# Kernel optimization log

Hardware: AMD Instinct MI355X
Metric: run time of the kernel (lower is better)

Reference implementation:

```python
import jax, jax.numpy as jnp
import numpy as np

D_MODEL = 1024
NUM_HEADS = 16
D_HEAD = D_MODEL // NUM_HEADS


def setup_inputs() -> dict:
    key = jax.random.key(0)
    kx, kq, kk, kv, ko = jax.random.split(key, 5)
    scale = 1.0 / np.sqrt(D_MODEL)
    X = jax.random.normal(kx, (4, 2048, D_MODEL), dtype=jnp.float32)
    # nn.Linear weights stored as [out, in]; we keep that convention.
    W_Q = jax.random.uniform(kq, (D_MODEL, D_MODEL), jnp.float32, -scale, scale)
    W_K = jax.random.uniform(kk, (D_MODEL, D_MODEL), jnp.float32, -scale, scale)
    W_V = jax.random.uniform(kv, (D_MODEL, D_MODEL), jnp.float32, -scale, scale)
    W_O = jax.random.uniform(ko, (D_MODEL, D_MODEL), jnp.float32, -scale, scale)
    return {"X": X, "W_Q": W_Q, "W_K": W_K, "W_V": W_V, "W_O": W_O}


def reference(X, W_Q, W_K, W_V, W_O):
    B, S, D = X.shape
    H, Dh = NUM_HEADS, D_HEAD
    # projections (Linear: x @ W.T)
    Q = (X @ W_Q.T).reshape(B, S, H, Dh).transpose(0, 2, 1, 3)  # [B,H,S,Dh]
    K = (X @ W_K.T).reshape(B, S, H, Dh).transpose(0, 2, 1, 3)
    V = (X @ W_V.T).reshape(B, S, H, Dh).transpose(0, 2, 1, 3)
    scores = jnp.einsum('bhqd,bhkd->bhqk', Q, K) / jnp.sqrt(jnp.float32(Dh))
    causal = jnp.tril(jnp.ones((S, S), dtype=bool))  # True = keep
    scores = jnp.where(causal, scores, -jnp.inf)
    attn = jax.nn.softmax(scores, axis=-1)
    out = jnp.einsum('bhqk,bhkd->bhqd', attn, V)  # [B,H,S,Dh]
    out = out.transpose(0, 2, 1, 3).reshape(B, S, D)
    return out @ W_O.T
```

## Files before the change

### kernel.cpp

```cpp
#include <hip/hip_runtime.h>

#define S_LEN 2048
#define NH 16
#define DH 64
#define DM 1024
#define M_TOK 8192
#define SZX ((size_t)M_TOK * DM)
#define SZW ((size_t)DM * DM)

typedef unsigned short u16;
typedef unsigned int u32;
typedef __attribute__((ext_vector_type(8))) short bf16x8;
typedef __attribute__((ext_vector_type(4))) float f32x4;

__device__ __forceinline__ u16 f2bf(float f) {
  union { float f; u32 u; } v; v.f = f;
  return (u16)((v.u + 0x8000u) >> 16);
}
__device__ __forceinline__ u32 pack_bf2(float x, float y) {
  union { float f; u32 u; } a, b; a.f = x; b.f = y;
  return __builtin_amdgcn_perm(b.u + 0x8000u, a.u + 0x8000u, 0x07060302u);
}
__device__ __forceinline__ float fast_exp2(float x) {
  float r; asm("v_exp_f32 %0, %1" : "=v"(r) : "v"(x)); return r;
}
__device__ __forceinline__ void gload16(const u16* g, u16* l) {
  __builtin_amdgcn_global_load_lds((const __attribute__((address_space(1))) void*)g,
                                   (__attribute__((address_space(3))) void*)l,
                                   16, 0, 0);
}

#define QSCALE 0.18033688f

__global__ __launch_bounds__(256) void cast_all(const float* __restrict__ X,
                                                const float* __restrict__ q,
                                                const float* __restrict__ k,
                                                const float* __restrict__ v,
                                                const float* __restrict__ o,
                                                u16* __restrict__ dst) {
  const int i = (blockIdx.x * 256 + threadIdx.x) * 8;
  const float* src;
  int local;
  if (i < (int)SZX) { src = X; local = i; }
  else {
    const int j = i - (int)SZX;
    const int region = j >> 20;
    src = (region == 0) ? q : (region == 1) ? k : (region == 2) ? v : o;
    local = j & ((1 << 20) - 1);
  }
  const float4 a = *(const float4*)(src + local);
  const float4 b = *(const float4*)(src + local + 4);
  uint4 r;
  r.x = pack_bf2(a.x, a.y); r.y = pack_bf2(a.z, a.w);
  r.z = pack_bf2(b.x, b.y); r.w = pack_bf2(b.z, b.w);
  *(uint4*)(dst + i) = r;
}

template<int MODE>
__global__ __launch_bounds__(256) void gemm128(const u16* __restrict__ A,
                                               const u16* __restrict__ Bw,
                                               void* __restrict__ Cv) {
  __shared__ __align__(16) u16 As[128 * 64];
  __shared__ __align__(16) u16 Bs[128 * 64];
  const int tid = threadIdx.x;
  const int lane = tid & 63;
  const int wave = tid >> 6;
  const int col = lane & 15, quad = lane >> 4;
  const int wm = (wave & 1) * 64, wn = (wave >> 1) * 64;
  const int m_blk = blockIdx.x * 128, n_blk = blockIdx.y * 128;

  const int srow = tid >> 3;
  const int skg = (tid & 7) ^ (srow & 7);
  const u16* Ag = A + (size_t)(m_blk + srow) * DM + skg * 8;
  const u16* Bg = Bw + (size_t)(n_blk + srow) * DM + skg * 8;

  f32x4 acc[4][4];
#pragma unroll
  for (int i = 0; i < 4; ++i)
#pragma unroll
    for (int j = 0; j < 4; ++j) acc[i][j] = (f32x4){0.f, 0.f, 0.f, 0.f};

  const int c0 = (quad ^ (col & 7)) * 8;
  const int c1 = c0 ^ 32;

  for (int k0 = 0; k0 < DM; k0 += 64) {
#pragma unroll
    for (int i = 0; i < 4; ++i) {
      gload16(Ag + (size_t)(32 * i) * DM + k0, &As[tid * 8 + i * 2048]);
      gload16(Bg + (size_t)(32 * i) * DM + k0, &Bs[tid * 8 + i * 2048]);
    }
    __syncthreads();
    bf16x8 af[4], bf[4];
#pragma unroll
    for (int i = 0; i < 4; ++i)
      af[i] = *(const bf16x8*)&As[(wm + i * 16 + col) * 64 + c0];
#pragma unroll
    for (int j = 0; j < 4; ++j)
      bf[j] = *(const bf16x8*)&Bs[(wn + j * 16 + col) * 64 + c0];
#pragma unroll
    for (int i = 0; i < 4; ++i)
#pragma unroll
      for (int j = 0; j < 4; ++j)
        acc[i][j] = __builtin_amdgcn_mfma_f32_16x16x32_bf16(af[i], bf[j], acc[i][j], 0, 0, 0);
#pragma unroll
    for (int i = 0; i < 4; ++i)
      af[i] = *(const bf16x8*)&As[(wm + i * 16 + col) * 64 + c1];
#pragma unroll
    for (int j = 0; j < 4; ++j)
      bf[j] = *(const bf16x8*)&Bs[(wn + j * 16 + col) * 64 + c1];
#pragma unroll
    for (int i = 0; i < 4; ++i)
#pragma unroll
      for (int j = 0; j < 4; ++j)
        acc[i][j] = __builtin_amdgcn_mfma_f32_16x16x32_bf16(af[i], bf[j], acc[i][j], 0, 0, 0);
    __syncthreads();
  }

#pragma unroll
  for (int i = 0; i < 4; ++i) {
#pragma unroll
    for (int j = 0; j < 4; ++j) {
      const int n = n_blk + wn + j * 16 + col;
      if (MODE == 0) {
        const int which = n >> 10;
        const int nn = n & 1023;
        const int h = nn >> 6, dh = nn & 63;
        u16* dst = (u16*)Cv + (size_t)which * SZX;
        const int m0 = m_blk + wm + i * 16 + quad * 4;
        const int b = m0 >> 11;
        if (which == 2) {
          uint2 pk;
          pk.x = pack_bf2(acc[i][j][0], acc[i][j][1]);
          pk.y = pack_bf2(acc[i][j][2], acc[i][j][3]);
          *(uint2*)&dst[((size_t)((b * NH + h) * DH + dh)) * S_LEN + (m0 & 2047)] = pk;
        } else {
          const float sc = (which == 0) ? QSCALE : 1.0f;
#pragma unroll
          for (int r = 0; r < 4; ++r) {
            const int m = m0 + r, s = m & 2047;
            dst[((size_t)(b * NH + h) * S_LEN + s) * DH + dh] = f2bf(acc[i][j][r] * sc);
          }
        }
      } else {
#pragma unroll
        for (int r = 0; r < 4; ++r) {
          const int m = m_blk + wm + i * 16 + quad * 4 + r;
          ((float*)Cv)[(size_t)m * DM + n] = acc[i][j][r];
        }
      }
    }
  }
}

template<bool DIAG_H, bool DIAG_L, bool WITH_L>
__device__ __forceinline__ void stepHL(const u16* __restrict__ Ksb,
                                       const u16* __restrict__ Vsb,
                                       u16* __restrict__ Pw,
                                       bf16x8 qH0, bf16x8 qH1,
                                       bf16x8 qL0, bf16x8 qL1,
                                       f32x4& lH, f32x4* oH,
                                       f32x4& lL, f32x4* oL,
                                       f32x4 zero4, bf16x8 ones,
                                       int c0, int c1, int col, int quad,
                                       int q_l) {
  const int colc = col & 7;
  f32x4 sH[4], sL[4];
#pragma unroll
  for (int t = 0; t < 4; ++t) {
    const int row = (t * 16 + col) * 64;
    const bf16x8 kf0 = *(const bf16x8*)&Ksb[row + c0];
    const bf16x8 kf1 = *(const bf16x8*)&Ksb[row + c1];
    f32x4 z = __builtin_amdgcn_mfma_f32_16x16x32_bf16(kf0, qH0, zero4, 0, 0, 0);
    sH[t] = __builtin_amdgcn_mfma_f32_16x16x32_bf16(kf1, qH1, z, 0, 0, 0);
    if (WITH_L) {
      f32x4 y = __builtin_amdgcn_mfma_f32_16x16x32_bf16(kf0, qL0, zero4, 0, 0, 0);
      sL[t] = __builtin_amdgcn_mfma_f32_16x16x32_bf16(kf1, qL1, y, 0, 0, 0);
    }
  }
#pragma unroll
  for (int t = 0; t < 4; ++t)
#pragma unroll
    for (int r = 0; r < 4; ++r) {
      if (DIAG_H && (t * 16 + quad * 4 + r) > q_l) sH[t][r] = -1e30f;
      sH[t][r] = fast_exp2(sH[t][r]);
      if (WITH_L) {
        if (DIAG_L && (t * 16 + quad * 4 + r) > q_l) sL[t][r] = -1e30f;
        sL[t][r] = fast_exp2(sL[t][r]);
      }
    }
#pragma unroll
  for (int t = 0; t < 4; ++t) {
    uint2 pk;
    pk.x = pack_bf2(sH[t][0], sH[t][1]);
    pk.y = pack_bf2(sH[t][2], sH[t][3]);
    const int pg = (((t * 2) + (quad >> 1)) ^ colc) * 8 + (quad & 1) * 4;
    *(uint2*)&Pw[col * 64 + pg] = pk;
  }
  {
    const bf16x8 pf0 = *(const bf16x8*)&Pw[col * 64 + ((quad ^ colc) * 8)];
    const bf16x8 pf1 = *(const bf16x8*)&Pw[col * 64 + (((4 + quad) ^ colc) * 8)];
    lH = __builtin_amdgcn_mfma_f32_16x16x32_bf16(ones, pf0, lH, 0, 0, 0);
    lH = __builtin_amdgcn_mfma_f32_16x16x32_bf16(ones, pf1, lH, 0, 0, 0);
#pragma unroll
    for (int t = 0; t < 4; ++t) {
      const int row = (t * 16 + col) * 64;
      const bf16x8 vf0 = *(const bf16x8*)&Vsb[row + c0];
      const bf16x8 vf1 = *(const bf16x8*)&Vsb[row + c1];
      oH[t] = __builtin_amdgcn_mfma_f32_16x16x32_bf16(vf0, pf0, oH[t], 0, 0, 0);
      oH[t] = __builtin_amdgcn_mfma_f32_16x16x32_bf16(vf1, pf1, oH[t], 0, 0, 0);
    }
  }
  if (WITH_L) {
#pragma unroll
    for (int t = 0; t < 4; ++t) {
      uint2 pk;
      pk.x = pack_bf2(sL[t][0], sL[t][1]);
      pk.y = pack_bf2(sL[t][2], sL[t][3]);
      const int pg = (((t * 2) + (quad >> 1)) ^ colc) * 8 + (quad & 1) * 4;
      *(uint2*)&Pw[col * 64 + pg] = pk;
    }
    const bf16x8 pf0 = *(const bf16x8*)&Pw[col * 64 + ((quad ^ colc) * 8)];
    const bf16x8 pf1 = *(const bf16x8*)&Pw[col * 64 + (((4 + quad) ^ colc) * 8)];
    lL = __builtin_amdgcn_mfma_f32_16x16x32_bf16(ones, pf0, lL, 0, 0, 0);
    lL = __builtin_amdgcn_mfma_f32_16x16x32_bf16(ones, pf1, lL, 0, 0, 0);
#pragma unroll
    for (int t = 0; t < 4; ++t) {
      const int row = (t * 16 + col) * 64;
      const bf16x8 vf0 = *(const bf16x8*)&Vsb[row + c0];
      const bf16x8 vf1 = *(const bf16x8*)&Vsb[row + c1];
      oL[t] = __builtin_amdgcn_mfma_f32_16x16x32_bf16(vf0, pf0, oL[t], 0, 0, 0);
      oL[t] = __builtin_amdgcn_mfma_f32_16x16x32_bf16(vf1, pf1, oL[t], 0, 0, 0);
    }
  }
}

__global__ __launch_bounds__(256) void attn_kernel(const u16* __restrict__ Qg,
                                                   const u16* __restrict__ Kg,
                                                   const u16* __restrict__ Vtg,
                                                   u16* __restrict__ AO) {
  __shared__ __align__(16) u16 Ks[2][64 * 64];
  __shared__ __align__(16) u16 Vs[2][64 * 64];
  __shared__ __align__(16) u16 Ps[4][16 * 64];

  const int id = blockIdx.x;
  const int k9 = id >> 3;
  const int qtH = 16 + (k9 & 15);
  const int qtL = 31 - qtH;
  const int bh = ((id & 7) << 3) | (k9 >> 4);
  const int tid = threadIdx.x, lane = tid & 63, wave = tid >> 6;
  const int col = lane & 15, quad = lane >> 4;

  const u16* Qb = Qg + (size_t)bh * S_LEN * DH;
  const u16* Kb = Kg + (size_t)bh * S_LEN * DH;
  const u16* Vb = Vtg + (size_t)bh * DH * S_LEN;

  const u16* qrowH = Qb + (size_t)(qtH * 64 + wave * 16 + col) * DH + quad * 8;
  const u16* qrowL = Qb + (size_t)(qtL * 64 + wave * 16 + col) * DH + quad * 8;
  const bf16x8 qH0 = *(const bf16x8*)(qrowH);
  const bf16x8 qH1 = *(const bf16x8*)(qrowH + 32);
  const bf16x8 qL0 = *(const bf16x8*)(qrowL);
  const bf16x8 qL1 = *(const bf16x8*)(qrowL + 32);

  const f32x4 zero4 = (f32x4){0.f, 0.f, 0.f, 0.f};
  const bf16x8 ones = (bf16x8){0x3F80, 0x3F80, 0x3F80, 0x3F80,
                               0x3F80, 0x3F80, 0x3F80, 0x3F80};

  f32x4 lH = zero4, lL = zero4;
  f32x4 oH[4], oL[4];
#pragma unroll
  for (int t = 0; t < 4; ++t) { oH[t] = zero4; oL[t] = zero4; }

  const int sr0 = tid >> 3;
  const int sk0 = (tid & 7) ^ (sr0 & 7);
  const u16* K0 = Kb + (size_t)sr0 * DH + sk0 * 8;
  const u16* K1 = Kb + (size_t)(sr0 + 32) * DH + sk0 * 8;
  const u16* V0 = Vb + (size_t)sr0 * S_LEN + sk0 * 8;
  const u16* V1 = Vb + (size_t)(sr0 + 32) * S_LEN + sk0 * 8;

  const int c0 = (quad ^ (col & 7)) * 8;
  const int c1 = c0 ^ 32;
  const int q_l = wave * 16 + col;
  u16* Pw = &Ps[wave][0];

  gload16(K0, &Ks[0][tid * 8]);
  gload16(K1, &Ks[0][2048 + tid * 8]);
  gload16(V0, &Vs[0][tid * 8]);
  gload16(V1, &Vs[0][2048 + tid * 8]);

#define PREFETCH(nk) do {                                   \
    const int nb_ = (nk) & 1;                               \
    gload16(K0 + (size_t)(nk) * 64 * DH, &Ks[nb_][tid * 8]);\
    gload16(K1 + (size_t)(nk) * 64 * DH, &Ks[nb_][2048 + tid * 8]); \
    gload16(V0 + (nk) * 64, &Vs[nb_][tid * 8]);             \
    gload16(V1 + (nk) * 64, &Vs[nb_][2048 + tid * 8]);      \
  } while (0)

  int kt = 0;
  for (; kt < qtL; ++kt) {
    __syncthreads();
    PREFETCH(kt + 1);
    stepHL<false, false, true>(&Ks[kt & 1][0], &Vs[kt & 1][0], Pw,
                               qH0, qH1, qL0, qL1, lH, oH, lL, oL,
                               zero4, ones, c0, c1, col, quad, q_l);
  }
  {
    __syncthreads();
    PREFETCH(kt + 1);
    stepHL<false, true, true>(&Ks[kt & 1][0], &Vs[kt & 1][0], Pw,
                              qH0, qH1, qL0, qL1, lH, oH, lL, oL,
                              zero4, ones, c0, c1, col, quad, q_l);
    ++kt;
  }
  for (; kt < qtH; ++kt) {
    __syncthreads();
    PREFETCH(kt + 1);
    stepHL<false, false, false>(&Ks[kt & 1][0], &Vs[kt & 1][0], Pw,
                                qH0, qH1, qL0, qL1, lH, oH, lL, oL,
                                zero4, ones, c0, c1, col, quad, q_l);
  }
  {
    __syncthreads();
    stepHL<true, false, false>(&Ks[kt & 1][0], &Vs[kt & 1][0], Pw,
                               qH0, qH1, qL0, qL1, lH, oH, lL, oL,
                               zero4, ones, c0, c1, col, quad, q_l);
  }
#undef PREFETCH

  const int b = bh >> 4, h = bh & 15;
  {
    const float inv = __builtin_amdgcn_rcpf(lH[0]);
    const size_t base = (size_t)(b * S_LEN + qtH * 64 + q_l) * DM + h * DH;
#pragma unroll
    for (int t = 0; t < 4; ++t) {
      uint2 pk;
      pk.x = pack_bf2(oH[t][0] * inv, oH[t][1] * inv);
      pk.y = pack_bf2(oH[t][2] * inv, oH[t][3] * inv);
      *(uint2*)&AO[base + t * 16 + quad * 4] = pk;
    }
  }
  {
    const float inv = __builtin_amdgcn_rcpf(lL[0]);
    const size_t base = (size_t)(b * S_LEN + qtL * 64 + q_l) * DM + h * DH;
#pragma unroll
    for (int t = 0; t < 4; ++t) {
      uint2 pk;
      pk.x = pack_bf2(oL[t][0] * inv, oL[t][1] * inv);
      pk.y = pack_bf2(oL[t][2] * inv, oL[t][3] * inv);
      *(uint2*)&AO[base + t * 16 + quad * 4] = pk;
    }
  }
}

extern "C" void kernel_launch(void* const* d_in, const int* in_sizes, int n_in,
                              void* d_out, int out_size, void* d_ws, size_t ws_size,
                              hipStream_t stream) {
  const float* X  = (const float*)d_in[0];
  const float* Wq = (const float*)d_in[1];
  const float* Wk = (const float*)d_in[2];
  const float* Wv = (const float*)d_in[3];
  const float* Wo = (const float*)d_in[4];

  u16* Xb   = (u16*)d_ws;
  u16* Wqkv = Xb + SZX;
  u16* Wob  = Wqkv + 3 * SZW;
  u16* Qb   = Wob + SZW;
  u16* Kb   = Qb + SZX;
  u16* VT   = Kb + SZX;
  u16* AO   = Xb;

  cast_all<<<(int)((SZX + 4 * SZW) / 8 / 256), 256, 0, stream>>>(X, Wq, Wk, Wv, Wo, Xb);

  gemm128<0><<<dim3(M_TOK / 128, 3 * DM / 128), 256, 0, stream>>>(Xb, Wqkv, Qb);

  attn_kernel<<<dim3(1024), 256, 0, stream>>>(Qb, Kb, VT, AO);

  gemm128<1><<<dim3(M_TOK / 128, DM / 128), 256, 0, stream>>>(AO, Wob, d_out);
}
```

Measured before the change: 245.5 us.

## Add 256x256 double-buffered 8-wave GEMM for fused QKV projection

Replaces the 128x128 tile QKV projection GEMM with a new 256x256 tile kernel using 512 threads. It double-buffers LDS and interleaves global-to-LDS staging with four MFMA sub-phases under s_setprio. The larger tile raises arithmetic intensity and cuts global traffic, and the software pipeline is meant to hide load latency. In exchange it uses 128KB of LDS per block and heavy register pressure, and it launches only 384 blocks, which may hurt occupancy and load balance.

```diff
diff --git a/kernel.cpp b/kernel.cpp
--- a/kernel.cpp
+++ b/kernel.cpp
@@ -7,6 +7,7 @@
 #define M_TOK 8192
 #define SZX ((size_t)M_TOK * DM)
 #define SZW ((size_t)DM * DM)
+#define NT 16
 
 typedef unsigned short u16;
 typedef unsigned int u32;
@@ -54,6 +55,154 @@
   r.x = pack_bf2(a.x, a.y); r.y = pack_bf2(a.z, a.w);
   r.z = pack_bf2(b.x, b.y); r.w = pack_bf2(b.z, b.w);
   *(uint4*)(dst + i) = r;
+}
+
+template<int QM, int QN>
+__device__ __forceinline__ void mm_phase(f32x4 (&acc)[8][4],
+                                         const bf16x8 (&A)[4][2],
+                                         const bf16x8 (&B)[2][2]) {
+  __builtin_amdgcn_s_setprio(1);
+#pragma unroll
+  for (int i = 0; i < 4; ++i)
+#pragma unroll
+    for (int j = 0; j < 2; ++j) {
+      f32x4& d = acc[QM * 4 + i][QN * 2 + j];
+      d = __builtin_amdgcn_mfma_f32_16x16x32_bf16(A[i][0], B[j][0], d, 0, 0, 0);
+      d = __builtin_amdgcn_mfma_f32_16x16x32_bf16(A[i][1], B[j][1], d, 0, 0, 0);
+    }
+  __builtin_amdgcn_s_setprio(0);
+}
+
+__global__ __launch_bounds__(512, 2) void gemm256_qkv(const u16* __restrict__ A,
+                                                      const u16* __restrict__ Bw,
+                                                      u16* __restrict__ Cv) {
+  __shared__ __align__(16) u16 As[2][256 * 64];
+  __shared__ __align__(16) u16 Bs[2][256 * 64];
+  const int tid = threadIdx.x;
+  const int lane = tid & 63;
+  const int wave = tid >> 6;
+  const int col = lane & 15, quad = lane >> 4;
+  const int wr = wave >> 2;
+  const int wc = wave & 3;
+  const int m_blk = blockIdx.x * 256, n_blk = blockIdx.y * 256;
+
+  const int srow = tid >> 3;
+  const int skg = (tid & 7) ^ (srow & 7);
+  const int lofs = tid * 8;
+  const u16* Ag = A + (size_t)(m_blk + srow) * DM + skg * 8;
+  const u16* Bg = Bw + (size_t)(n_blk + srow) * DM + skg * 8;
+
+  f32x4 acc[8][4];
+#pragma unroll
+  for (int i = 0; i < 8; ++i)
+#pragma unroll
+    for (int j = 0; j < 4; ++j) acc[i][j] = (f32x4){0.f, 0.f, 0.f, 0.f};
+
+  const int c0 = (quad ^ (col & 7)) * 8;
+  const int c1 = c0 ^ 32;
+
+#define STG_A(hm, tt) do {                                                   \
+    gload16(Ag + (size_t)((hm) * 128) * DM + (tt) * 64,                      \
+            &As[(tt) & 1][(hm) * 8192 + lofs]);                              \
+    gload16(Ag + (size_t)((hm) * 128 + 64) * DM + (tt) * 64,                 \
+            &As[(tt) & 1][(hm) * 8192 + 4096 + lofs]);                       \
+  } while (0)
+#define STG_B(hn, tt) do {                                                   \
+    gload16(Bg + (size_t)((hn) * 128) * DM + (tt) * 64,                      \
+            &Bs[(tt) & 1][(hn) * 8192 + lofs]);                              \
+    gload16(Bg + (size_t)((hn) * 128 + 64) * DM + (tt) * 64,                 \
+            &Bs[(tt) & 1][(hn) * 8192 + 4096 + lofs]);                       \
+  } while (0)
+
+  STG_A(0, 0); STG_B(0, 0); STG_A(1, 0); STG_B(1, 0);
+  STG_A(0, 1); STG_B(0, 1);
+  asm volatile("s_waitcnt vmcnt(4)" ::: "memory");
+  __builtin_amdgcn_s_barrier();
+
+  bf16x8 af[4][2], bq0[2][2], bq1[2][2];
+
+  for (int t = 0; t < NT; ++t) {
+    const u16* Ab = As[t & 1];
+    const u16* Bb = Bs[t & 1];
+
+#pragma unroll
+    for (int i = 0; i < 4; ++i) {
+      const int ro = (wr * 64 + i * 16 + col) * 64;
+      af[i][0] = *(const bf16x8*)&Ab[ro + c0];
+      af[i][1] = *(const bf16x8*)&Ab[ro + c1];
+    }
+#pragma unroll
+    for (int j = 0; j < 2; ++j) {
+      const int ro = (wc * 32 + j * 16 + col) * 64;
+      bq0[j][0] = *(const bf16x8*)&Bb[ro + c0];
+      bq0[j][1] = *(const bf16x8*)&Bb[ro + c1];
+    }
+    if (t + 1 < NT) STG_A(1, t + 1);
+    __builtin_amdgcn_s_barrier();
+    asm volatile("s_waitcnt lgkmcnt(0)" ::: "memory");
+    mm_phase<0, 0>(acc, af, bq0);
+    __builtin_amdgcn_s_barrier();
+
+#pragma unroll
+    for (int j = 0; j < 2; ++j) {
+      const int ro = (128 + wc * 32 + j * 16 + col) * 64;
+      bq1[j][0] = *(const bf16x8*)&Bb[ro + c0];
+      bq1[j][1] = *(const bf16x8*)&Bb[ro + c1];
+    }
+    if (t + 1 < NT) STG_B(1, t + 1);
+    __builtin_amdgcn_s_barrier();
+    asm volatile("s_waitcnt lgkmcnt(0)" ::: "memory");
+    mm_phase<0, 1>(acc, af, bq1);
+    __builtin_amdgcn_s_barrier();
+
+#pragma unroll
+    for (int i = 0; i < 4; ++i) {
+      const int ro = (128 + wr * 64 + i * 16 + col) * 64;
+      af[i][0] = *(const bf16x8*)&Ab[ro + c0];
+      af[i][1] = *(const bf16x8*)&Ab[ro + c1];
+    }
+    if (t + 2 < NT) STG_A(0, t + 2);
+    __builtin_amdgcn_s_barrier();
+    asm volatile("s_waitcnt lgkmcnt(0)" ::: "memory");
+    mm_phase<1, 0>(acc, af, bq0);
+    __builtin_amdgcn_s_barrier();
+
+    if (t + 2 < NT) STG_B(0, t + 2);
+    __builtin_amdgcn_s_barrier();
+    mm_phase<1, 1>(acc, af, bq1);
+    if (t < NT - 2) { asm volatile("s_waitcnt vmcnt(4)" ::: "memory"); }
+    else            { asm volatile("s_waitcnt vmcnt(0)" ::: "memory"); }
+    __builtin_amdgcn_s_barrier();
+  }
+#undef STG_A
+#undef STG_B
+
+  const int which = n_blk >> 10;
+#pragma unroll
+  for (int mi = 0; mi < 8; ++mi) {
+#pragma unroll
+    for (int nj = 0; nj < 4; ++nj) {
+      const int n = n_blk + (nj >> 1) * 128 + wc * 32 + (nj & 1) * 16 + col;
+      const int nn = n & 1023;
+      const int h = nn >> 6, dh = nn & 63;
+      u16* dst = Cv + (size_t)which * SZX;
+      const int m0 = m_blk + (mi >> 2) * 128 + wr * 64 + (mi & 3) * 16 + quad * 4;
+      const int b = m0 >> 11;
+      if (which == 2) {
+        uint2 pk;
+        pk.x = pack_bf2(acc[mi][nj][0], acc[mi][nj][1]);
+        pk.y = pack_bf2(acc[mi][nj][2], acc[mi][nj][3]);
+        *(uint2*)&dst[((size_t)((b * NH + h) * DH + dh)) * S_LEN + (m0 & 2047)] = pk;
+      } else {
+        const float sc = (which == 0) ? QSCALE : 1.0f;
+#pragma unroll
+        for (int r = 0; r < 4; ++r) {
+          const int m = m0 + r, s = m & 2047;
+          dst[((size_t)(b * NH + h) * S_LEN + s) * DH + dh] = f2bf(acc[mi][nj][r] * sc);
+        }
+      }
+    }
+  }
 }
 
 template<int MODE>
@@ -370,7 +519,7 @@
 
   cast_all<<<(int)((SZX + 4 * SZW) / 8 / 256), 256, 0, stream>>>(X, Wq, Wk, Wv, Wo, Xb);
 
-  gemm128<0><<<dim3(M_TOK / 128, 3 * DM / 128), 256, 0, stream>>>(Xb, Wqkv, Qb);
+  gemm256_qkv<<<dim3(M_TOK / 256, 3 * DM / 256), 512, 0, stream>>>(Xb, Wqkv, Qb);
 
   attn_kernel<<<dim3(1024), 256, 0, stream>>>(Qb, Kb, VT, AO);
 
```

After: 255.0 us. 3.8% more time.

## Pair adjacent query tiles per K/V stream, two pairs per block

Applied to the files above, without the earlier changes.

Each attention block now processes two pairs of adjacent query tiles (2p, 2p+1), taken from mirrored positions so the causal work is balanced. The two tiles in a pair share nearly the whole K/V stream, so each loaded K/V tile feeds both query tiles, and the lower tile is fully masked only on the final step. The grid is halved to 512 blocks. The old H/L pairing (qtH, 31-qtH) also shared K/V across the lower tile's prefix. The new layout aims for better MFMA interleaving (H and L PV MFMAs are now issued together), at the cost of fewer blocks and a serialized second pass per block.

```diff
diff --git a/kernel.cpp b/kernel.cpp
--- a/kernel.cpp
+++ b/kernel.cpp
@@ -152,17 +152,17 @@
   }
 }
 
-template<bool DIAG_H, bool DIAG_L, bool WITH_L>
-__device__ __forceinline__ void stepHL(const u16* __restrict__ Ksb,
-                                       const u16* __restrict__ Vsb,
-                                       u16* __restrict__ Pw,
-                                       bf16x8 qH0, bf16x8 qH1,
-                                       bf16x8 qL0, bf16x8 qL1,
-                                       f32x4& lH, f32x4* oH,
-                                       f32x4& lL, f32x4* oL,
-                                       f32x4 zero4, bf16x8 ones,
-                                       int c0, int c1, int col, int quad,
-                                       int q_l) {
+template<bool DIAG_L>
+__device__ __forceinline__ void stepM(const u16* __restrict__ Ksb,
+                                      const u16* __restrict__ Vsb,
+                                      u16* __restrict__ Pw,
+                                      bf16x8 qH0, bf16x8 qH1,
+                                      bf16x8 qL0, bf16x8 qL1,
+                                      f32x4& lH, f32x4* oH,
+                                      f32x4& lL, f32x4* oL,
+                                      f32x4 zero4, bf16x8 ones,
+                                      int c0, int c1, int col, int quad,
+                                      int q_l) {
   const int colc = col & 7;
   f32x4 sH[4], sL[4];
 #pragma unroll
@@ -172,21 +172,16 @@
     const bf16x8 kf1 = *(const bf16x8*)&Ksb[row + c1];
     f32x4 z = __builtin_amdgcn_mfma_f32_16x16x32_bf16(kf0, qH0, zero4, 0, 0, 0);
     sH[t] = __builtin_amdgcn_mfma_f32_16x16x32_bf16(kf1, qH1, z, 0, 0, 0);
-    if (WITH_L) {
-      f32x4 y = __builtin_amdgcn_mfma_f32_16x16x32_bf16(kf0, qL0, zero4, 0, 0, 0);
-      sL[t] = __builtin_amdgcn_mfma_f32_16x16x32_bf16(kf1, qL1, y, 0, 0, 0);
-    }
+    f32x4 y = __builtin_amdgcn_mfma_f32_16x16x32_bf16(kf0, qL0, zero4, 0, 0, 0);
+    sL[t] = __builtin_amdgcn_mfma_f32_16x16x32_bf16(kf1, qL1, y, 0, 0, 0);
   }
 #pragma unroll
   for (int t = 0; t < 4; ++t)
 #pragma unroll
     for (int r = 0; r < 4; ++r) {
-      if (DIAG_H && (t * 16 + quad * 4 + r) > q_l) sH[t][r] = -1e30f;
       sH[t][r] = fast_exp2(sH[t][r]);
-      if (WITH_L) {
-        if (DIAG_L && (t * 16 + quad * 4 + r) > q_l) sL[t][r] = -1e30f;
-        sL[t][r] = fast_exp2(sL[t][r]);
-      }
+      if (DIAG_L && (t * 16 + quad * 4 + r) > q_l) sL[t][r] = -1e30f;
+      sL[t][r] = fast_exp2(sL[t][r]);
     }
 #pragma unroll
   for (int t = 0; t < 4; ++t) {
@@ -196,41 +191,79 @@
     const int pg = (((t * 2) + (quad >> 1)) ^ colc) * 8 + (quad & 1) * 4;
     *(uint2*)&Pw[col * 64 + pg] = pk;
   }
-  {
-    const bf16x8 pf0 = *(const bf16x8*)&Pw[col * 64 + ((quad ^ colc) * 8)];
-    const bf16x8 pf1 = *(const bf16x8*)&Pw[col * 64 + (((4 + quad) ^ colc) * 8)];
-    lH = __builtin_amdgcn_mfma_f32_16x16x32_bf16(ones, pf0, lH, 0, 0, 0);
-    lH = __builtin_amdgcn_mfma_f32_16x16x32_bf16(ones, pf1, lH, 0, 0, 0);
-#pragma unroll
-    for (int t = 0; t < 4; ++t) {
-      const int row = (t * 16 + col) * 64;
-      const bf16x8 vf0 = *(const bf16x8*)&Vsb[row + c0];
-      const bf16x8 vf1 = *(const bf16x8*)&Vsb[row + c1];
-      oH[t] = __builtin_amdgcn_mfma_f32_16x16x32_bf16(vf0, pf0, oH[t], 0, 0, 0);
-      oH[t] = __builtin_amdgcn_mfma_f32_16x16x32_bf16(vf1, pf1, oH[t], 0, 0, 0);
-    }
-  }
-  if (WITH_L) {
-#pragma unroll
-    for (int t = 0; t < 4; ++t) {
-      uint2 pk;
-      pk.x = pack_bf2(sL[t][0], sL[t][1]);
-      pk.y = pack_bf2(sL[t][2], sL[t][3]);
-      const int pg = (((t * 2) + (quad >> 1)) ^ colc) * 8 + (quad & 1) * 4;
-      *(uint2*)&Pw[col * 64 + pg] = pk;
-    }
-    const bf16x8 pf0 = *(const bf16x8*)&Pw[col * 64 + ((quad ^ colc) * 8)];
-    const bf16x8 pf1 = *(const bf16x8*)&Pw[col * 64 + (((4 + quad) ^ colc) * 8)];
-    lL = __builtin_amdgcn_mfma_f32_16x16x32_bf16(ones, pf0, lL, 0, 0, 0);
-    lL = __builtin_amdgcn_mfma_f32_16x16x32_bf16(ones, pf1, lL, 0, 0, 0);
-#pragma unroll
-    for (int t = 0; t < 4; ++t) {
-      const int row = (t * 16 + col) * 64;
-      const bf16x8 vf0 = *(const bf16x8*)&Vsb[row + c0];
-      const bf16x8 vf1 = *(const bf16x8*)&Vsb[row + c1];
-      oL[t] = __builtin_amdgcn_mfma_f32_16x16x32_bf16(vf0, pf0, oL[t], 0, 0, 0);
-      oL[t] = __builtin_amdgcn_mfma_f32_16x16x32_bf16(vf1, pf1, oL[t], 0, 0, 0);
-    }
+  const bf16x8 pfH0 = *(const bf16x8*)&Pw[col * 64 + ((quad ^ colc) * 8)];
+  const bf16x8 pfH1 = *(const bf16x8*)&Pw[col * 64 + (((4 + quad) ^ colc) * 8)];
+#pragma unroll
+  for (int t = 0; t < 4; ++t) {
+    uint2 pk;
+    pk.x = pack_bf2(sL[t][0], sL[t][1]);
+    pk.y = pack_bf2(sL[t][2], sL[t][3]);
+    const int pg = (((t * 2) + (quad >> 1)) ^ colc) * 8 + (quad & 1) * 4;
+    *(uint2*)&Pw[col * 64 + pg] = pk;
+  }
+  const bf16x8 pfL0 = *(const bf16x8*)&Pw[col * 64 + ((quad ^ colc) * 8)];
+  const bf16x8 pfL1 = *(const bf16x8*)&Pw[col * 64 + (((4 + quad) ^ colc) * 8)];
+  lH = __builtin_amdgcn_mfma_f32_16x16x32_bf16(ones, pfH0, lH, 0, 0, 0);
+  lH = __builtin_amdgcn_mfma_f32_16x16x32_bf16(ones, pfH1, lH, 0, 0, 0);
+  lL = __builtin_amdgcn_mfma_f32_16x16x32_bf16(ones, pfL0, lL, 0, 0, 0);
+  lL = __builtin_amdgcn_mfma_f32_16x16x32_bf16(ones, pfL1, lL, 0, 0, 0);
+#pragma unroll
+  for (int t = 0; t < 4; ++t) {
+    const int row = (t * 16 + col) * 64;
+    const bf16x8 vf0 = *(const bf16x8*)&Vsb[row + c0];
+    const bf16x8 vf1 = *(const bf16x8*)&Vsb[row + c1];
+    oH[t] = __builtin_amdgcn_mfma_f32_16x16x32_bf16(vf0, pfH0, oH[t], 0, 0, 0);
+    oH[t] = __builtin_amdgcn_mfma_f32_16x16x32_bf16(vf1, pfH1, oH[t], 0, 0, 0);
+    oL[t] = __builtin_amdgcn_mfma_f32_16x16x32_bf16(vf0, pfL0, oL[t], 0, 0, 0);
+    oL[t] = __builtin_amdgcn_mfma_f32_16x16x32_bf16(vf1, pfL1, oL[t], 0, 0, 0);
+  }
+}
+
+template<bool DIAG_H>
+__device__ __forceinline__ void stepS(const u16* __restrict__ Ksb,
+                                      const u16* __restrict__ Vsb,
+                                      u16* __restrict__ Pw,
+                                      bf16x8 qH0, bf16x8 qH1,
+                                      f32x4& lH, f32x4* oH,
+                                      f32x4 zero4, bf16x8 ones,
+                                      int c0, int c1, int col, int quad,
+                                      int q_l) {
+  const int colc = col & 7;
+  f32x4 sH[4];
+#pragma unroll
+  for (int t = 0; t < 4; ++t) {
+    const int row = (t * 16 + col) * 64;
+    const bf16x8 kf0 = *(const bf16x8*)&Ksb[row + c0];
+    const bf16x8 kf1 = *(const bf16x8*)&Ksb[row + c1];
+    f32x4 z = __builtin_amdgcn_mfma_f32_16x16x32_bf16(kf0, qH0, zero4, 0, 0, 0);
+    sH[t] = __builtin_amdgcn_mfma_f32_16x16x32_bf16(kf1, qH1, z, 0, 0, 0);
+  }
+#pragma unroll
+  for (int t = 0; t < 4; ++t)
+#pragma unroll
+    for (int r = 0; r < 4; ++r) {
+      if (DIAG_H && (t * 16 + quad * 4 + r) > q_l) sH[t][r] = -1e30f;
+      sH[t][r] = fast_exp2(sH[t][r]);
+    }
+#pragma unroll
+  for (int t = 0; t < 4; ++t) {
+    uint2 pk;
+    pk.x = pack_bf2(sH[t][0], sH[t][1]);
+    pk.y = pack_bf2(sH[t][2], sH[t][3]);
+    const int pg = (((t * 2) + (quad >> 1)) ^ colc) * 8 + (quad & 1) * 4;
+    *(uint2*)&Pw[col * 64 + pg] = pk;
+  }
+  const bf16x8 pf0 = *(const bf16x8*)&Pw[col * 64 + ((quad ^ colc) * 8)];
+  const bf16x8 pf1 = *(const bf16x8*)&Pw[col * 64 + (((4 + quad) ^ colc) * 8)];
+  lH = __builtin_amdgcn_mfma_f32_16x16x32_bf16(ones, pf0, lH, 0, 0, 0);
+  lH = __builtin_amdgcn_mfma_f32_16x16x32_bf16(ones, pf1, lH, 0, 0, 0);
+#pragma unroll
+  for (int t = 0; t < 4; ++t) {
+    const int row = (t * 16 + col) * 64;
+    const bf16x8 vf0 = *(const bf16x8*)&Vsb[row + c0];
+    const bf16x8 vf1 = *(const bf16x8*)&Vsb[row + c1];
+    oH[t] = __builtin_amdgcn_mfma_f32_16x16x32_bf16(vf0, pf0, oH[t], 0, 0, 0);
+    oH[t] = __builtin_amdgcn_mfma_f32_16x16x32_bf16(vf1, pf1, oH[t], 0, 0, 0);
   }
 }
 
@@ -243,10 +276,8 @@
   __shared__ __align__(16) u16 Ps[4][16 * 64];
 
   const int id = blockIdx.x;
-  const int k9 = id >> 3;
-  const int qtH = 16 + (k9 & 15);
-  const int qtL = 31 - qtH;
-  const int bh = ((id & 7) << 3) | (k9 >> 4);
+  const int bh = ((id & 7) << 3) | (id >> 6);
+  const int slot = (id >> 3) & 7;
   const int tid = threadIdx.x, lane = tid & 63, wave = tid >> 6;
   const int col = lane & 15, quad = lane >> 4;
 
@@ -254,21 +285,9 @@
   const u16* Kb = Kg + (size_t)bh * S_LEN * DH;
   const u16* Vb = Vtg + (size_t)bh * DH * S_LEN;
 
-  const u16* qrowH = Qb + (size_t)(qtH * 64 + wave * 16 + col) * DH + quad * 8;
-  const u16* qrowL = Qb + (size_t)(qtL * 64 + wave * 16 + col) * DH + quad * 8;
-  const bf16x8 qH0 = *(const bf16x8*)(qrowH);
-  const bf16x8 qH1 = *(const bf16x8*)(qrowH + 32);
-  const bf16x8 qL0 = *(const bf16x8*)(qrowL);
-  const bf16x8 qL1 = *(const bf16x8*)(qrowL + 32);
-
   const f32x4 zero4 = (f32x4){0.f, 0.f, 0.f, 0.f};
   const bf16x8 ones = (bf16x8){0x3F80, 0x3F80, 0x3F80, 0x3F80,
                                0x3F80, 0x3F80, 0x3F80, 0x3F80};
-
-  f32x4 lH = zero4, lL = zero4;
-  f32x4 oH[4], oL[4];
-#pragma unroll
-  for (int t = 0; t < 4; ++t) { oH[t] = zero4; oL[t] = zero4; }
 
   const int sr0 = tid >> 3;
   const int sk0 = (tid & 7) ^ (sr0 & 7);
@@ -281,11 +300,7 @@
   const int c1 = c0 ^ 32;
   const int q_l = wave * 16 + col;
   u16* Pw = &Ps[wave][0];
-
-  gload16(K0, &Ks[0][tid * 8]);
-  gload16(K1, &Ks[0][2048 + tid * 8]);
-  gload16(V0, &Vs[0][tid * 8]);
-  gload16(V1, &Vs[0][2048 + tid * 8]);
+  const int b = bh >> 4, h = bh & 15;
 
 #define PREFETCH(nk) do {                                   \
     const int nb_ = (nk) & 1;                               \
@@ -295,60 +310,73 @@
     gload16(V1 + (nk) * 64, &Vs[nb_][2048 + tid * 8]);      \
   } while (0)
 
-  int kt = 0;
-  for (; kt < qtL; ++kt) {
+  for (int pi = 0; pi < 2; ++pi) {
+    const int p = pi ? slot : (15 - slot);
+    const int qtH = 2 * p + 1, qtL = 2 * p;
+
+    const u16* qrowH = Qb + (size_t)(qtH * 64 + wave * 16 + col) * DH + quad * 8;
+    const bf16x8 qH0 = *(const bf16x8*)(qrowH);
+    const bf16x8 qH1 = *(const bf16x8*)(qrowH + 32);
+    const bf16x8 qL0 = *(const bf16x8*)(qrowH - 64 * DH);
+    const bf16x8 qL1 = *(const bf16x8*)(qrowH - 64 * DH + 32);
+
+    f32x4 lH = zero4, lL = zero4;
+    f32x4 oH[4], oL[4];
+#pragma unroll
+    for (int t = 0; t < 4; ++t) { oH[t] = zero4; oL[t] = zero4; }
+
     __syncthreads();
-    PREFETCH(kt + 1);
-    stepHL<false, false, true>(&Ks[kt & 1][0], &Vs[kt & 1][0], Pw,
-                               qH0, qH1, qL0, qL1, lH, oH, lL, oL,
-                               zero4, ones, c0, c1, col, quad, q_l);
-  }
-  {
-    __syncthreads();
-    PREFETCH(kt + 1);
-    stepHL<false, true, true>(&Ks[kt & 1][0], &Vs[kt & 1][0], Pw,
-                              qH0, qH1, qL0, qL1, lH, oH, lL, oL,
-                              zero4, ones, c0, c1, col, quad, q_l);
-    ++kt;
-  }
-  for (; kt < qtH; ++kt) {
-    __syncthreads();
-    PREFETCH(kt + 1);
-    stepHL<false, false, false>(&Ks[kt & 1][0], &Vs[kt & 1][0], Pw,
-                                qH0, qH1, qL0, qL1, lH, oH, lL, oL,
-                                zero4, ones, c0, c1, col, quad, q_l);
-  }
-  {
-    __syncthreads();
-    stepHL<true, false, false>(&Ks[kt & 1][0], &Vs[kt & 1][0], Pw,
-                               qH0, qH1, qL0, qL1, lH, oH, lL, oL,
-                               zero4, ones, c0, c1, col, quad, q_l);
+    gload16(K0, &Ks[0][tid * 8]);
+    gload16(K1, &Ks[0][2048 + tid * 8]);
+    gload16(V0, &Vs[0][tid * 8]);
+    gload16(V1, &Vs[0][2048 + tid * 8]);
+
+    int kt = 0;
+    for (; kt < qtL; ++kt) {
+      __syncthreads();
+      PREFETCH(kt + 1);
+      stepM<false>(&Ks[kt & 1][0], &Vs[kt & 1][0], Pw,
+                   qH0, qH1, qL0, qL1, lH, oH, lL, oL,
+                   zero4, ones, c0, c1, col, quad, q_l);
+    }
+    {
+      __syncthreads();
+      PREFETCH(kt + 1);
+      stepM<true>(&Ks[kt & 1][0], &Vs[kt & 1][0], Pw,
+                  qH0, qH1, qL0, qL1, lH, oH, lL, oL,
+                  zero4, ones, c0, c1, col, quad, q_l);
+      ++kt;
+    }
+    {
+      __syncthreads();
+      stepS<true>(&Ks[kt & 1][0], &Vs[kt & 1][0], Pw,
+                  qH0, qH1, lH, oH, zero4, ones, c0, c1, col, quad, q_l);
+    }
+
+    {
+      const float inv = __builtin_amdgcn_rcpf(lH[0]);
+      const size_t base = (size_t)(b * S_LEN + qtH * 64 + q_l) * DM + h * DH;
+#pragma unroll
+      for (int t = 0; t < 4; ++t) {
+        uint2 pk;
+        pk.x = pack_bf2(oH[t][0] * inv, oH[t][1] * inv);
+        pk.y = pack_bf2(oH[t][2] * inv, oH[t][3] * inv);
+        *(uint2*)&AO[base + t * 16 + quad * 4] = pk;
+      }
+    }
+    {
+      const float inv = __builtin_amdgcn_rcpf(lL[0]);
+      const size_t base = (size_t)(b * S_LEN + qtL * 64 + q_l) * DM + h * DH;
+#pragma unroll
+      for (int t = 0; t < 4; ++t) {
+        uint2 pk;
+        pk.x = pack_bf2(oL[t][0] * inv, oL[t][1] * inv);
+        pk.y = pack_bf2(oL[t][2] * inv, oL[t][3] * inv);
+        *(uint2*)&AO[base + t * 16 + quad * 4] = pk;
+      }
+    }
   }
 #undef PREFETCH
-
-  const int b = bh >> 4, h = bh & 15;
-  {
-    const float inv = __builtin_amdgcn_rcpf(lH[0]);
-    const size_t base = (size_t)(b * S_LEN + qtH * 64 + q_l) * DM + h * DH;
-#pragma unroll
-    for (int t = 0; t < 4; ++t) {
-      uint2 pk;
-      pk.x = pack_bf2(oH[t][0] * inv, oH[t][1] * inv);
-      pk.y = pack_bf2(oH[t][2] * inv, oH[t][3] * inv);
-      *(uint2*)&AO[base + t * 16 + quad * 4] = pk;
-    }
-  }
-  {
-    const float inv = __builtin_amdgcn_rcpf(lL[0]);
-    const size_t base = (size_t)(b * S_LEN + qtL * 64 + q_l) * DM + h * DH;
-#pragma unroll
-    for (int t = 0; t < 4; ++t) {
-      uint2 pk;
-      pk.x = pack_bf2(oL[t][0] * inv, oL[t][1] * inv);
-      pk.y = pack_bf2(oL[t][2] * inv, oL[t][3] * inv);
-      *(uint2*)&AO[base + t * 16 + quad * 4] = pk;
-    }
-  }
 }
 
 extern "C" void kernel_launch(void* const* d_in, const int* in_sizes, int n_in,
@@ -372,7 +400,7 @@
 
   gemm128<0><<<dim3(M_TOK / 128, 3 * DM / 128), 256, 0, stream>>>(Xb, Wqkv, Qb);
 
-  attn_kernel<<<dim3(1024), 256, 0, stream>>>(Qb, Kb, VT, AO);
+  attn_kernel<<<dim3(512), 256, 0, stream>>>(Qb, Kb, VT, AO);
 
   gemm128<1><<<dim3(M_TOK / 128, DM / 128), 256, 0, stream>>>(AO, Wob, d_out);
 }
```

After: 237.1 us. 3.4% less time.
